# Kernel tuning notes

Hardware: AMD Instinct MI355X
Metric: run time of the kernel (lower is better)

## Reference

```python
import jax, jax.numpy as jnp
import numpy as np

HIDDEN = 1024
HEADS = 16
HEAD_DIM = HIDDEN // HEADS

def setup_inputs() -> dict:
    key = jax.random.key(0)
    k1, k2, k3 = jax.random.split(key, 3)
    scale = 1.0 / np.sqrt(HIDDEN)
    return {
        "x": jax.random.normal(k1, (2, 2048, HIDDEN), dtype=jnp.float32),
        "w_qkv": jax.random.normal(k2, (HIDDEN, 3 * HIDDEN), dtype=jnp.float32) * scale,
        "b_qkv": jnp.zeros((3 * HIDDEN,), dtype=jnp.float32),
        "w_out": jax.random.normal(k3, (HIDDEN, HIDDEN), dtype=jnp.float32) * scale,
        "b_out": jnp.zeros((HIDDEN,), dtype=jnp.float32),
    }

def reference(x, w_qkv, b_qkv, w_out, b_out):
    B, S, H = x.shape
    qkv = x @ w_qkv + b_qkv                              # (B,S,3H)
    qkv = qkv.reshape(B, S, 3, HEADS, HEAD_DIM)
    qkv = jnp.transpose(qkv, (2, 0, 3, 1, 4))            # (3,B,nh,S,hd)
    q, k, v = qkv[0], qkv[1], qkv[2]
    scores = jnp.einsum("bhqd,bhkd->bhqk", q, k) / np.sqrt(HEAD_DIM)
    causal = jnp.triu(jnp.ones((S, S), dtype=bool), k=1)  # True above diagonal
    scores = jnp.where(causal, -jnp.inf, scores)
    attn = jax.nn.softmax(scores, axis=-1)               # dropout: eval mode (identity)
    out = jnp.einsum("bhqk,bhkd->bhqd", attn, v)
    out = jnp.transpose(out, (0, 2, 1, 3)).reshape(B, S, H)
    return out @ w_out + b_out
```

## Files before the change

kernel.cpp:

```cpp
#include <hip/hip_runtime.h>
#include <hip/hip_bf16.h>

typedef short short8 __attribute__((ext_vector_type(8)));
typedef float f32x4 __attribute__((ext_vector_type(4)));
typedef unsigned int uint4v __attribute__((ext_vector_type(4)));

typedef const __attribute__((address_space(1))) unsigned int* gas_ptr;
typedef __attribute__((address_space(3))) unsigned int* las_ptr;
#define ASYNC16(g, l) __builtin_amdgcn_global_load_lds((gas_ptr)(g), (las_ptr)(l), 16, 0, 0)

__device__ __forceinline__ unsigned short f2bf(float f) {
    unsigned int u = __builtin_bit_cast(unsigned int, f);
    u += 0x7fff + ((u >> 16) & 1);
    return (unsigned short)(u >> 16);
}
__device__ __forceinline__ float bf2f(unsigned short s) {
    unsigned int u = (unsigned int)s << 16;
    return __builtin_bit_cast(float, u);
}
__device__ __forceinline__ unsigned int pkbf_trunc(float lo, float hi) {
    return __builtin_amdgcn_perm(__builtin_bit_cast(unsigned int, hi),
                                 __builtin_bit_cast(unsigned int, lo), 0x07060302u);
}
__device__ __forceinline__ float fexp2(float x) {
#if __has_builtin(__builtin_amdgcn_exp2f)
    return __builtin_amdgcn_exp2f(x);
#else
    return __expf(x * 0.6931471805599453f);
#endif
}

__device__ __forceinline__ void transpose_tile(
    const float* __restrict__ w, unsigned short* __restrict__ wt,
    int K, int N, int k0, int n0, unsigned short* tile)
{
    for (int i = threadIdx.x; i < 64 * 64; i += 256) {
        int r = i >> 6, c = i & 63;
        tile[r * 65 + c] = f2bf(w[(size_t)(k0 + r) * N + n0 + c]);
    }
    __syncthreads();
    for (int i = threadIdx.x; i < 64 * 64; i += 256) {
        int r = i >> 6, c = i & 63;
        wt[(size_t)(n0 + r) * K + k0 + c] = tile[c * 65 + r];
    }
}

__global__ __launch_bounds__(256) void prep(
    const float* __restrict__ x, const float* __restrict__ w_qkv,
    const float* __restrict__ w_out,
    unsigned short* __restrict__ x_b, unsigned short* __restrict__ wqkv_t,
    unsigned short* __restrict__ wout_t)
{
    __shared__ unsigned short tile[64 * 65];
    int bid = blockIdx.x;
    if (bid < 4096) {
        int i = (bid * 256 + threadIdx.x) * 4;
        float4 v = *(const float4*)(x + i);
        ushort4 o;
        o.x = f2bf(v.x); o.y = f2bf(v.y); o.z = f2bf(v.z); o.w = f2bf(v.w);
        *(ushort4*)(x_b + i) = o;
    } else if (bid < 4096 + 768) {
        int t = bid - 4096;
        transpose_tile(w_qkv, wqkv_t, 1024, 3072, (t / 48) * 64, (t % 48) * 64, tile);
    } else {
        int t = bid - 4864;
        transpose_tile(w_out, wout_t, 1024, 1024, (t >> 4) * 64, (t & 15) * 64, tile);
    }
}


template<bool OUT_BF16, bool QKV>
__global__ __launch_bounds__(256, 3) void gemm_bt(
    const unsigned short* __restrict__ A,
    const unsigned short* __restrict__ Bt,
    const float* __restrict__ bias,
    void* __restrict__ C,
    unsigned short* __restrict__ vTp,
    int M, int N, int K)
{
    __shared__ __align__(16) unsigned short As[2][128 * 32];
    __shared__ __align__(16) unsigned short Bs[2][128 * 32];
    const int tid = threadIdx.x;
    const int lane = tid & 63;
    const int wave = tid >> 6;
    const int wr = wave >> 1, wc = wave & 1;
    const int m0 = blockIdx.x * 128, n0 = blockIdx.y * 128;
    const int fr = lane & 15, fq = lane >> 4;

    f32x4 acc[4][4] = {};

    const int grow = lane >> 2;
    const int gcol = (lane & 3) * 8;
    const unsigned short* Ag = A  + (size_t)(m0 + wave * 32 + grow) * K + gcol;
    const unsigned short* Bg = Bt + (size_t)(n0 + wave * 32 + grow) * K + gcol;
    const int wb0 = (wave * 32) * 32;
    const int wb1 = (wave * 32 + 16) * 32;

    for (int k0 = 0; k0 < K; k0 += 64) {
        __syncthreads();
        ASYNC16(Ag + k0,               As[0] + wb0);
        ASYNC16(Ag + 16 * K + k0,      As[0] + wb1);
        ASYNC16(Bg + k0,               Bs[0] + wb0);
        ASYNC16(Bg + 16 * K + k0,      Bs[0] + wb1);
        ASYNC16(Ag + k0 + 32,          As[1] + wb0);
        ASYNC16(Ag + 16 * K + k0 + 32, As[1] + wb1);
        ASYNC16(Bg + k0 + 32,          Bs[1] + wb0);
        ASYNC16(Bg + 16 * K + k0 + 32, Bs[1] + wb1);
        __syncthreads();

#pragma unroll
        for (int h = 0; h < 2; h++) {
            short8 af[4], bfr[4];
#pragma unroll
            for (int i = 0; i < 4; i++)
                af[i] = *(const short8*)(As[h] + (wr * 64 + i * 16 + fr) * 32 + fq * 8);
#pragma unroll
            for (int j = 0; j < 4; j++)
                bfr[j] = *(const short8*)(Bs[h] + (wc * 64 + j * 16 + fr) * 32 + fq * 8);
#pragma unroll
            for (int i = 0; i < 4; i++)
#pragma unroll
                for (int j = 0; j < 4; j++)
                    acc[i][j] = __builtin_amdgcn_mfma_f32_16x16x32_bf16(af[i], bfr[j], acc[i][j], 0, 0, 0);
        }
    }

#pragma unroll
    for (int i = 0; i < 4; i++)
#pragma unroll
        for (int j = 0; j < 4; j++) {
            int col = n0 + wc * 64 + j * 16 + fr;
            float bv = bias[col];
            if (QKV && col >= 2048) {
                int hh = (col - 2048) >> 6, d = col & 63;
#pragma unroll
                for (int r = 0; r < 4; r++) {
                    int row = m0 + wr * 64 + i * 16 + fq * 4 + r;
                    int bb = row >> 11, s = row & 2047;
                    vTp[((size_t)(bb * 16 + hh) * 64 + d) * 2048 + s] = f2bf(acc[i][j][r] + bv);
                }
            } else {
                const int cstride = QKV ? 2048 : N;
#pragma unroll
                for (int r = 0; r < 4; r++) {
                    int row = m0 + wr * 64 + i * 16 + fq * 4 + r;
                    float v = acc[i][j][r] + bv;
                    if (OUT_BF16)
                        ((unsigned short*)C)[(size_t)row * cstride + col] = f2bf(v);
                    else
                        ((float*)C)[(size_t)row * cstride + col] = v;
                }
            }
        }
}


template<int RG0>
__device__ __forceinline__ void attn_step(
    const unsigned short* __restrict__ Ks0, const unsigned short* __restrict__ Ks1,
    const unsigned short* __restrict__ Vs0, const unsigned short* __restrict__ Vs1,
    unsigned short* __restrict__ Psw,
    const short8 (&qf)[2][2], const short8 ones,
    f32x4 (&o_acc)[2][4], f32x4 (&l_acc)[2],
    int j0, int fr, int fq,
    const int (&qrow0)[2], bool diagA, bool diagB)
{
    const int kpos = ((fq + (fr >> 1)) & 3) * 8;
    short8 kf[4][2];
#pragma unroll
    for (int t = 0; t < 4; t++) {
        kf[t][0] = *(const short8*)(Ks0 + (t * 16 + fr) * 32 + kpos);
        kf[t][1] = *(const short8*)(Ks1 + (t * 16 + fr) * 32 + kpos);
    }

    const float C1 = 0.18033688011112042f;
    const float C2 = -11.541560327111707f;

#pragma unroll
    for (int rg = RG0; rg < 2; rg++) {
        f32x4 s[4];
        __builtin_amdgcn_s_setprio(1);
#pragma unroll
        for (int t = 0; t < 4; t++) {
            s[t] = (f32x4){0.f, 0.f, 0.f, 0.f};
            s[t] = __builtin_amdgcn_mfma_f32_16x16x32_bf16(kf[t][0], qf[rg][0], s[t], 0, 0, 0);
            s[t] = __builtin_amdgcn_mfma_f32_16x16x32_bf16(kf[t][1], qf[rg][1], s[t], 0, 0, 0);
        }
        __builtin_amdgcn_s_setprio(0);
        const bool diag = (rg == 0) ? diagA : diagB;
        unsigned short* prow = Psw + rg * (16 * 64);
        const int qr = qrow0[rg] + fr;
        if (diag) {
#pragma unroll
            for (int t = 0; t < 4; t++) {
                const int kb = j0 + t * 16 + fq * 4;
                float p[4];
#pragma unroll
                for (int r = 0; r < 4; r++) {
                    float v = fexp2(s[t][r] * C1 + C2);
                    if (kb + r > qr) v = 0.f;
                    p[r] = v;
                }
                uint2 pk;
                pk.x = pkbf_trunc(p[0], p[1]);
                pk.y = pkbf_trunc(p[2], p[3]);
                const int blk = (t * 2 + (fq >> 1) + fr) & 7;
                *(uint2*)(prow + fr * 64 + blk * 8 + (fq & 1) * 4) = pk;
            }
        } else {
#pragma unroll
            for (int t = 0; t < 4; t++) {
                float p[4];
#pragma unroll
                for (int r = 0; r < 4; r++)
                    p[r] = fexp2(s[t][r] * C1 + C2);
                uint2 pk;
                pk.x = pkbf_trunc(p[0], p[1]);
                pk.y = pkbf_trunc(p[2], p[3]);
                const int blk = (t * 2 + (fq >> 1) + fr) & 7;
                *(uint2*)(prow + fr * 64 + blk * 8 + (fq & 1) * 4) = pk;
            }
        }
    }

#pragma unroll
    for (int ks = 0; ks < 2; ks++) {
        const unsigned short* Vsb = ks ? Vs1 : Vs0;
        const int colp = ((ks * 4 + fq + fr) & 7) * 8;
        short8 pf[2];
#pragma unroll
        for (int rg = RG0; rg < 2; rg++)
            pf[rg] = *(const short8*)(Psw + rg * (16 * 64) + fr * 64 + colp);
        __builtin_amdgcn_s_setprio(1);
#pragma unroll
        for (int t = 0; t < 4; t++) {
            short8 vf = *(const short8*)(Vsb + (t * 16 + fr) * 32 + kpos);
#pragma unroll
            for (int rg = RG0; rg < 2; rg++)
                o_acc[rg][t] = __builtin_amdgcn_mfma_f32_16x16x32_bf16(pf[rg], vf, o_acc[rg][t], 0, 0, 0);
        }
#pragma unroll
        for (int rg = RG0; rg < 2; rg++)
            l_acc[rg] = __builtin_amdgcn_mfma_f32_16x16x32_bf16(pf[rg], ones, l_acc[rg], 0, 0, 0);
        __builtin_amdgcn_s_setprio(0);
    }
}

__global__ __launch_bounds__(256, 2) void flash_attn(
    const unsigned short* __restrict__ qkv,
    const unsigned short* __restrict__ vT,
    unsigned short* __restrict__ Opart,
    float* __restrict__ lpart)
{
    const int p = blockIdx.x;
    const int g = blockIdx.y;
    const int h = blockIdx.z & 15, b = blockIdx.z >> 4;
    const int tid = threadIdx.x, wave = tid >> 6, lane = tid & 63;
    const int fr = lane & 15, fq = lane >> 4;
    const size_t RS = 2048;

    const unsigned short* Qb = qkv + (size_t)b * 2048 * RS + h * 64;
    const unsigned short* Kb = Qb + 1024;
    const unsigned short* Vt = vT + (size_t)(b * 16 + h) * 64 * 2048;

    __shared__ __align__(16) unsigned short Ks[2][64 * 32];
    __shared__ __align__(16) unsigned short Vs[2][64 * 32];
    __shared__ __align__(16) unsigned short Ps[4][2 * 16 * 64];

    short8 qf[2][2];
    int qrow0[2];
#pragma unroll
    for (int rg = 0; rg < 2; rg++) {
        int qt = (rg == 0) ? p : (31 - p);
        qrow0[rg] = qt * 64 + wave * 16;
        const unsigned short* qrow = Qb + (size_t)(qrow0[rg] + fr) * RS;
        qf[rg][0] = *(const short8*)(qrow + fq * 8);
        qf[rg][1] = *(const short8*)(qrow + 32 + fq * 8);
    }
    short8 ones;
#pragma unroll
    for (int e = 0; e < 8; e++) ones[e] = (short)0x3F80;

    f32x4 o_acc[2][4] = {};
    f32x4 l_acc[2] = {};

    const int grow = lane >> 2;
    const int gswz = (((lane & 3) - (grow >> 1)) & 3) * 8;
    const unsigned short* Kg = Kb + (size_t)(wave * 16 + grow) * RS + gswz;
    const unsigned short* Vg = Vt + (size_t)(wave * 16 + grow) * 2048 + gswz;
    const int wb = wave * 16 * 32;

    unsigned short* dK0 = Ks[0] + wb + lane * 8;
    unsigned short* dK1 = Ks[1] + wb + lane * 8;
    unsigned short* dV0 = Vs[0] + wb + lane * 8;
    unsigned short* dV1 = Vs[1] + wb + lane * 8;

    const int mid = (p >= 8) ? 8 : (16 - p);
    const int lo = g ? mid : 0;
    const int hi = g ? (32 - p) : mid;

    {
        const int j0 = lo * 64;
        uint4v aK0 = *(const uint4v*)(Kg + (size_t)j0 * RS);
        uint4v aK1 = *(const uint4v*)(Kg + (size_t)j0 * RS + 32);
        uint4v aV0 = *(const uint4v*)(Vg + j0);
        uint4v aV1 = *(const uint4v*)(Vg + j0 + 32);
        *(uint4v*)dK0 = aK0;
        *(uint4v*)dK1 = aK1;
        *(uint4v*)dV0 = aV0;
        *(uint4v*)dV1 = aV1;
    }
    __syncthreads();

    for (int jt = lo; jt < hi; jt++) {
        const int j0 = jt * 64;
        const bool more = (jt + 1 < hi);
        const int j0n = more ? (j0 + 64) : j0;

        uint4v aK0 = *(const uint4v*)(Kg + (size_t)j0n * RS);
        uint4v aK1 = *(const uint4v*)(Kg + (size_t)j0n * RS + 32);
        uint4v aV0 = *(const uint4v*)(Vg + j0n);
        uint4v aV1 = *(const uint4v*)(Vg + j0n + 32);

        bool diagA = (jt == p), diagB = (jt == 31 - p);
        if (jt <= p)
            attn_step<0>(Ks[0], Ks[1], Vs[0], Vs[1], Ps[wave], qf, ones,
                         o_acc, l_acc, j0, fr, fq, qrow0, diagA, diagB);
        else
            attn_step<1>(Ks[0], Ks[1], Vs[0], Vs[1], Ps[wave], qf, ones,
                         o_acc, l_acc, j0, fr, fq, qrow0, diagA, diagB);

        __syncthreads();
        if (more) {
            *(uint4v*)dK0 = aK0;
            *(uint4v*)dK1 = aK1;
            *(uint4v*)dV0 = aV0;
            *(uint4v*)dV1 = aV1;
        }
        __syncthreads();
    }

    unsigned short* Og = Opart + (size_t)g * 4096 * 1024;
    float* lg = lpart + (size_t)g * 4096 * 16;
#pragma unroll
    for (int rg = 0; rg < 2; rg++) {
#pragma unroll
        for (int t = 0; t < 4; t++)
#pragma unroll
            for (int r = 0; r < 4; r++) {
                int row = qrow0[rg] + fq * 4 + r;
                Og[(size_t)(b * 2048 + row) * 1024 + h * 64 + t * 16 + fr] = f2bf(o_acc[rg][t][r]);
            }
        if (fr == 0) {
#pragma unroll
            for (int r = 0; r < 4; r++) {
                int row = qrow0[rg] + fq * 4 + r;
                lg[(size_t)(b * 2048 + row) * 16 + h] = l_acc[rg][r];
            }
        }
    }
}

__global__ __launch_bounds__(256) void reduce_attn(
    const unsigned short* __restrict__ Opart, const float* __restrict__ lpart,
    unsigned short* __restrict__ out)
{
    int i = (blockIdx.x * 256 + threadIdx.x) * 8;
    int row = i >> 10, h = (i & 1023) >> 6;
    float lsum = lpart[(size_t)row * 16 + h] + lpart[(size_t)4096 * 16 + row * 16 + h];
    float inv = 1.0f / lsum;
    ushort4 a0 = *(const ushort4*)(Opart + i);
    ushort4 a1 = *(const ushort4*)(Opart + i + 4);
    ushort4 b0 = *(const ushort4*)(Opart + (size_t)4096 * 1024 + i);
    ushort4 b1 = *(const ushort4*)(Opart + (size_t)4096 * 1024 + i + 4);
    ushort4 o0, o1;
    o0.x = f2bf((bf2f(a0.x) + bf2f(b0.x)) * inv);
    o0.y = f2bf((bf2f(a0.y) + bf2f(b0.y)) * inv);
    o0.z = f2bf((bf2f(a0.z) + bf2f(b0.z)) * inv);
    o0.w = f2bf((bf2f(a0.w) + bf2f(b0.w)) * inv);
    o1.x = f2bf((bf2f(a1.x) + bf2f(b1.x)) * inv);
    o1.y = f2bf((bf2f(a1.y) + bf2f(b1.y)) * inv);
    o1.z = f2bf((bf2f(a1.z) + bf2f(b1.z)) * inv);
    o1.w = f2bf((bf2f(a1.w) + bf2f(b1.w)) * inv);
    *(ushort4*)(out + i) = o0;
    *(ushort4*)(out + i + 4) = o1;
}

extern "C" void kernel_launch(void* const* d_in, const int* in_sizes, int n_in,
                              void* d_out, int out_size, void* d_ws, size_t ws_size,
                              hipStream_t stream) {
    const float* x      = (const float*)d_in[0];
    const float* w_qkv  = (const float*)d_in[1];
    const float* b_qkv  = (const float*)d_in[2];
    const float* w_out  = (const float*)d_in[3];
    const float* b_out  = (const float*)d_in[4];
    float* out = (float*)d_out;

    char* ws = (char*)d_ws;
    unsigned short* x_b    = (unsigned short*)(ws);
    unsigned short* wqkv_t = (unsigned short*)(ws + 8u  * 1024 * 1024);
    unsigned short* wout_t = (unsigned short*)(ws + 14u * 1024 * 1024);
    unsigned short* qkv    = (unsigned short*)(ws + 16u * 1024 * 1024);
    unsigned short* attn   = (unsigned short*)(ws + 32u * 1024 * 1024);
    unsigned short* vT     = (unsigned short*)(ws + 40u * 1024 * 1024);
    unsigned short* Opart  = (unsigned short*)(ws + 48u * 1024 * 1024);
    float*          lpart  = (float*)         (ws + 64u * 1024 * 1024);

    prep<<<5120, 256, 0, stream>>>(x, w_qkv, w_out, x_b, wqkv_t, wout_t);
    gemm_bt<true, true ><<<dim3(32, 24), 256, 0, stream>>>(x_b,  wqkv_t, b_qkv, qkv, vT, 4096, 3072, 1024);
    flash_attn<<<dim3(16, 2, 32), 256, 0, stream>>>(qkv, vT, Opart, lpart);
    reduce_attn<<<2048, 256, 0, stream>>>(Opart, lpart, attn);
    gemm_bt<false, false><<<dim3(32, 8),  256, 0, stream>>>(attn, wout_t, b_out, out, nullptr, 4096, 1024, 1024);
}
```

Before: 187.4 us.

## Fuse x bf16 conversion and attention-split reduction into GEMM A-operand loads

The GEMM A-tile loading now reads fp32 x directly and converts it to bf16 in registers. It also combines the two flash-attention partial outputs and normalises them by the summed l values before writing into LDS. This removes the x-conversion portion of prep and the separate reduce_attn kernel, cutting a launch and a bf16 round trip through global memory. The cost is that A loads become synchronous register loads instead of async global-to-LDS copies. The QKV GEMM (24 column blocks) re-converts x redundantly, and the output GEMM (8 column blocks) re-reads two partials plus l values and redoes the divide.

```diff
diff --git a/kernel.cpp b/kernel.cpp
--- a/kernel.cpp
+++ b/kernel.cpp
@@ -17,6 +17,9 @@
 __device__ __forceinline__ float bf2f(unsigned short s) {
     unsigned int u = (unsigned int)s << 16;
     return __builtin_bit_cast(float, u);
+}
+__device__ __forceinline__ unsigned int pack2bf(float lo, float hi) {
+    return (unsigned int)f2bf(lo) | ((unsigned int)f2bf(hi) << 16);
 }
 __device__ __forceinline__ unsigned int pkbf_trunc(float lo, float hi) {
     return __builtin_amdgcn_perm(__builtin_bit_cast(unsigned int, hi),
@@ -46,34 +49,26 @@
 }
 
 __global__ __launch_bounds__(256) void prep(
-    const float* __restrict__ x, const float* __restrict__ w_qkv,
-    const float* __restrict__ w_out,
-    unsigned short* __restrict__ x_b, unsigned short* __restrict__ wqkv_t,
-    unsigned short* __restrict__ wout_t)
+    const float* __restrict__ w_qkv, const float* __restrict__ w_out,
+    unsigned short* __restrict__ wqkv_t, unsigned short* __restrict__ wout_t)
 {
     __shared__ unsigned short tile[64 * 65];
     int bid = blockIdx.x;
-    if (bid < 4096) {
-        int i = (bid * 256 + threadIdx.x) * 4;
-        float4 v = *(const float4*)(x + i);
-        ushort4 o;
-        o.x = f2bf(v.x); o.y = f2bf(v.y); o.z = f2bf(v.z); o.w = f2bf(v.w);
-        *(ushort4*)(x_b + i) = o;
-    } else if (bid < 4096 + 768) {
-        int t = bid - 4096;
-        transpose_tile(w_qkv, wqkv_t, 1024, 3072, (t / 48) * 64, (t % 48) * 64, tile);
+    if (bid < 768) {
+        transpose_tile(w_qkv, wqkv_t, 1024, 3072, (bid / 48) * 64, (bid % 48) * 64, tile);
     } else {
-        int t = bid - 4864;
+        int t = bid - 768;
         transpose_tile(w_out, wout_t, 1024, 1024, (t >> 4) * 64, (t & 15) * 64, tile);
     }
 }
 
 
-template<bool OUT_BF16, bool QKV>
+template<int AMODE, bool OUT_BF16, bool QKV>
 __global__ __launch_bounds__(256, 3) void gemm_bt(
-    const unsigned short* __restrict__ A,
+    const void* __restrict__ Araw,
     const unsigned short* __restrict__ Bt,
     const float* __restrict__ bias,
+    const float* __restrict__ lp,
     void* __restrict__ C,
     unsigned short* __restrict__ vTp,
     int M, int N, int K)
@@ -91,21 +86,57 @@
 
     const int grow = lane >> 2;
     const int gcol = (lane & 3) * 8;
-    const unsigned short* Ag = A  + (size_t)(m0 + wave * 32 + grow) * K + gcol;
-    const unsigned short* Bg = Bt + (size_t)(n0 + wave * 32 + grow) * K + gcol;
+    const int lrow = wave * 32 + grow;
+    const unsigned short* Bg = Bt + (size_t)(n0 + lrow) * K + gcol;
     const int wb0 = (wave * 32) * 32;
     const int wb1 = (wave * 32 + 16) * 32;
 
     for (int k0 = 0; k0 < K; k0 += 64) {
         __syncthreads();
-        ASYNC16(Ag + k0,               As[0] + wb0);
-        ASYNC16(Ag + 16 * K + k0,      As[0] + wb1);
         ASYNC16(Bg + k0,               Bs[0] + wb0);
         ASYNC16(Bg + 16 * K + k0,      Bs[0] + wb1);
-        ASYNC16(Ag + k0 + 32,          As[1] + wb0);
-        ASYNC16(Ag + 16 * K + k0 + 32, As[1] + wb1);
         ASYNC16(Bg + k0 + 32,          Bs[1] + wb0);
         ASYNC16(Bg + 16 * K + k0 + 32, Bs[1] + wb1);
+#pragma unroll
+        for (int h2 = 0; h2 < 2; h2++) {
+            const int r  = lrow + h2 * 16;
+            const int gr = m0 + r;
+#pragma unroll
+            for (int tw = 0; tw < 2; tw++) {
+                const int cb = k0 + tw * 32 + gcol;
+                uint4v w;
+                if (AMODE == 1) {
+                    const float* Af = (const float*)Araw;
+                    const float* src = Af + (size_t)gr * K + cb;
+                    float4 v0 = *(const float4*)src;
+                    float4 v1 = *(const float4*)(src + 4);
+                    w[0] = pack2bf(v0.x, v0.y);
+                    w[1] = pack2bf(v0.z, v0.w);
+                    w[2] = pack2bf(v1.x, v1.y);
+                    w[3] = pack2bf(v1.z, v1.w);
+                } else {
+                    const unsigned short* O0 = (const unsigned short*)Araw;
+                    const unsigned short* O1 = O0 + (size_t)4096 * 1024;
+                    const int hcol = cb >> 6;
+                    float ls = lp[(size_t)gr * 16 + hcol]
+                             + lp[(size_t)4096 * 16 + gr * 16 + hcol];
+                    float inv = 1.0f / ls;
+                    ushort4 a0 = *(const ushort4*)(O0 + (size_t)gr * 1024 + cb);
+                    ushort4 a1 = *(const ushort4*)(O0 + (size_t)gr * 1024 + cb + 4);
+                    ushort4 b0 = *(const ushort4*)(O1 + (size_t)gr * 1024 + cb);
+                    ushort4 b1 = *(const ushort4*)(O1 + (size_t)gr * 1024 + cb + 4);
+                    w[0] = pack2bf((bf2f(a0.x) + bf2f(b0.x)) * inv,
+                                   (bf2f(a0.y) + bf2f(b0.y)) * inv);
+                    w[1] = pack2bf((bf2f(a0.z) + bf2f(b0.z)) * inv,
+                                   (bf2f(a0.w) + bf2f(b0.w)) * inv);
+                    w[2] = pack2bf((bf2f(a1.x) + bf2f(b1.x)) * inv,
+                                   (bf2f(a1.y) + bf2f(b1.y)) * inv);
+                    w[3] = pack2bf((bf2f(a1.z) + bf2f(b1.z)) * inv,
+                                   (bf2f(a1.w) + bf2f(b1.w)) * inv);
+                }
+                *(uint4v*)(As[tw] + r * 32 + gcol) = w;
+            }
+        }
         __syncthreads();
 
 #pragma unroll
@@ -361,31 +392,6 @@
     }
 }
 
-__global__ __launch_bounds__(256) void reduce_attn(
-    const unsigned short* __restrict__ Opart, const float* __restrict__ lpart,
-    unsigned short* __restrict__ out)
-{
-    int i = (blockIdx.x * 256 + threadIdx.x) * 8;
-    int row = i >> 10, h = (i & 1023) >> 6;
-    float lsum = lpart[(size_t)row * 16 + h] + lpart[(size_t)4096 * 16 + row * 16 + h];
-    float inv = 1.0f / lsum;
-    ushort4 a0 = *(const ushort4*)(Opart + i);
-    ushort4 a1 = *(const ushort4*)(Opart + i + 4);
-    ushort4 b0 = *(const ushort4*)(Opart + (size_t)4096 * 1024 + i);
-    ushort4 b1 = *(const ushort4*)(Opart + (size_t)4096 * 1024 + i + 4);
-    ushort4 o0, o1;
-    o0.x = f2bf((bf2f(a0.x) + bf2f(b0.x)) * inv);
-    o0.y = f2bf((bf2f(a0.y) + bf2f(b0.y)) * inv);
-    o0.z = f2bf((bf2f(a0.z) + bf2f(b0.z)) * inv);
-    o0.w = f2bf((bf2f(a0.w) + bf2f(b0.w)) * inv);
-    o1.x = f2bf((bf2f(a1.x) + bf2f(b1.x)) * inv);
-    o1.y = f2bf((bf2f(a1.y) + bf2f(b1.y)) * inv);
-    o1.z = f2bf((bf2f(a1.z) + bf2f(b1.z)) * inv);
-    o1.w = f2bf((bf2f(a1.w) + bf2f(b1.w)) * inv);
-    *(ushort4*)(out + i) = o0;
-    *(ushort4*)(out + i + 4) = o1;
-}
-
 extern "C" void kernel_launch(void* const* d_in, const int* in_sizes, int n_in,
                               void* d_out, int out_size, void* d_ws, size_t ws_size,
                               hipStream_t stream) {
@@ -397,18 +403,15 @@
     float* out = (float*)d_out;
 
     char* ws = (char*)d_ws;
-    unsigned short* x_b    = (unsigned short*)(ws);
     unsigned short* wqkv_t = (unsigned short*)(ws + 8u  * 1024 * 1024);
     unsigned short* wout_t = (unsigned short*)(ws + 14u * 1024 * 1024);
     unsigned short* qkv    = (unsigned short*)(ws + 16u * 1024 * 1024);
-    unsigned short* attn   = (unsigned short*)(ws + 32u * 1024 * 1024);
     unsigned short* vT     = (unsigned short*)(ws + 40u * 1024 * 1024);
     unsigned short* Opart  = (unsigned short*)(ws + 48u * 1024 * 1024);
     float*          lpart  = (float*)         (ws + 64u * 1024 * 1024);
 
-    prep<<<5120, 256, 0, stream>>>(x, w_qkv, w_out, x_b, wqkv_t, wout_t);
-    gemm_bt<true, true ><<<dim3(32, 24), 256, 0, stream>>>(x_b,  wqkv_t, b_qkv, qkv, vT, 4096, 3072, 1024);
+    prep<<<1024, 256, 0, stream>>>(w_qkv, w_out, wqkv_t, wout_t);
+    gemm_bt<1, true, true ><<<dim3(32, 24), 256, 0, stream>>>(x, wqkv_t, b_qkv, nullptr, qkv, vT, 4096, 3072, 1024);
     flash_attn<<<dim3(16, 2, 32), 256, 0, stream>>>(qkv, vT, Opart, lpart);
-    reduce_attn<<<2048, 256, 0, stream>>>(Opart, lpart, attn);
-    gemm_bt<false, false><<<dim3(32, 8),  256, 0, stream>>>(attn, wout_t, b_out, out, nullptr, 4096, 1024, 1024);
-}
+    gemm_bt<2, false, false><<<dim3(32, 8), 256, 0, stream>>>(Opart, wout_t, b_out, lpart, out, nullptr, 4096, 1024, 1024);
+}
```

Result: slower. 219.8 us (+17.3%).

## Remove split-KV partitioning and fuse normalization into flash attention epilogue

Applied to the files above, without the earlier changes.

Each attention block now processes the full causal key range for its paired query tiles instead of splitting it into two halves. The separate reduction kernel and the partial O/l buffers are removed, and the output is normalized by 1/l directly in the epilogue. This avoids the partial writes, the extra launch and the reduce pass, at the cost of half as many blocks and longer per-block serial loops.

```diff
diff --git a/kernel.cpp b/kernel.cpp
--- a/kernel.cpp
+++ b/kernel.cpp
@@ -249,12 +249,10 @@
 __global__ __launch_bounds__(256, 2) void flash_attn(
     const unsigned short* __restrict__ qkv,
     const unsigned short* __restrict__ vT,
-    unsigned short* __restrict__ Opart,
-    float* __restrict__ lpart)
+    unsigned short* __restrict__ attn)
 {
     const int p = blockIdx.x;
-    const int g = blockIdx.y;
-    const int h = blockIdx.z & 15, b = blockIdx.z >> 4;
+    const int h = blockIdx.y & 15, b = blockIdx.y >> 4;
     const int tid = threadIdx.x, wave = tid >> 6, lane = tid & 63;
     const int fr = lane & 15, fq = lane >> 4;
     const size_t RS = 2048;
@@ -295,16 +293,13 @@
     unsigned short* dV0 = Vs[0] + wb + lane * 8;
     unsigned short* dV1 = Vs[1] + wb + lane * 8;
 
-    const int mid = (p >= 8) ? 8 : (16 - p);
-    const int lo = g ? mid : 0;
-    const int hi = g ? (32 - p) : mid;
+    const int hi = 32 - p;
 
     {
-        const int j0 = lo * 64;
-        uint4v aK0 = *(const uint4v*)(Kg + (size_t)j0 * RS);
-        uint4v aK1 = *(const uint4v*)(Kg + (size_t)j0 * RS + 32);
-        uint4v aV0 = *(const uint4v*)(Vg + j0);
-        uint4v aV1 = *(const uint4v*)(Vg + j0 + 32);
+        uint4v aK0 = *(const uint4v*)(Kg);
+        uint4v aK1 = *(const uint4v*)(Kg + 32);
+        uint4v aV0 = *(const uint4v*)(Vg);
+        uint4v aV1 = *(const uint4v*)(Vg + 32);
         *(uint4v*)dK0 = aK0;
         *(uint4v*)dK1 = aK1;
         *(uint4v*)dV0 = aV0;
@@ -312,7 +307,7 @@
     }
     __syncthreads();
 
-    for (int jt = lo; jt < hi; jt++) {
+    for (int jt = 0; jt < hi; jt++) {
         const int j0 = jt * 64;
         const bool more = (jt + 1 < hi);
         const int j0n = more ? (j0 + 64) : j0;
@@ -340,50 +335,21 @@
         __syncthreads();
     }
 
-    unsigned short* Og = Opart + (size_t)g * 4096 * 1024;
-    float* lg = lpart + (size_t)g * 4096 * 16;
 #pragma unroll
     for (int rg = 0; rg < 2; rg++) {
+        float inv[4];
+#pragma unroll
+        for (int r = 0; r < 4; r++)
+            inv[r] = 1.0f / l_acc[rg][r];
 #pragma unroll
         for (int t = 0; t < 4; t++)
 #pragma unroll
             for (int r = 0; r < 4; r++) {
                 int row = qrow0[rg] + fq * 4 + r;
-                Og[(size_t)(b * 2048 + row) * 1024 + h * 64 + t * 16 + fr] = f2bf(o_acc[rg][t][r]);
+                attn[(size_t)(b * 2048 + row) * 1024 + h * 64 + t * 16 + fr] =
+                    f2bf(o_acc[rg][t][r] * inv[r]);
             }
-        if (fr == 0) {
-#pragma unroll
-            for (int r = 0; r < 4; r++) {
-                int row = qrow0[rg] + fq * 4 + r;
-                lg[(size_t)(b * 2048 + row) * 16 + h] = l_acc[rg][r];
-            }
-        }
-    }
-}
-
-__global__ __launch_bounds__(256) void reduce_attn(
-    const unsigned short* __restrict__ Opart, const float* __restrict__ lpart,
-    unsigned short* __restrict__ out)
-{
-    int i = (blockIdx.x * 256 + threadIdx.x) * 8;
-    int row = i >> 10, h = (i & 1023) >> 6;
-    float lsum = lpart[(size_t)row * 16 + h] + lpart[(size_t)4096 * 16 + row * 16 + h];
-    float inv = 1.0f / lsum;
-    ushort4 a0 = *(const ushort4*)(Opart + i);
-    ushort4 a1 = *(const ushort4*)(Opart + i + 4);
-    ushort4 b0 = *(const ushort4*)(Opart + (size_t)4096 * 1024 + i);
-    ushort4 b1 = *(const ushort4*)(Opart + (size_t)4096 * 1024 + i + 4);
-    ushort4 o0, o1;
-    o0.x = f2bf((bf2f(a0.x) + bf2f(b0.x)) * inv);
-    o0.y = f2bf((bf2f(a0.y) + bf2f(b0.y)) * inv);
-    o0.z = f2bf((bf2f(a0.z) + bf2f(b0.z)) * inv);
-    o0.w = f2bf((bf2f(a0.w) + bf2f(b0.w)) * inv);
-    o1.x = f2bf((bf2f(a1.x) + bf2f(b1.x)) * inv);
-    o1.y = f2bf((bf2f(a1.y) + bf2f(b1.y)) * inv);
-    o1.z = f2bf((bf2f(a1.z) + bf2f(b1.z)) * inv);
-    o1.w = f2bf((bf2f(a1.w) + bf2f(b1.w)) * inv);
-    *(ushort4*)(out + i) = o0;
-    *(ushort4*)(out + i + 4) = o1;
+    }
 }
 
 extern "C" void kernel_launch(void* const* d_in, const int* in_sizes, int n_in,
@@ -403,12 +369,9 @@
     unsigned short* qkv    = (unsigned short*)(ws + 16u * 1024 * 1024);
     unsigned short* attn   = (unsigned short*)(ws + 32u * 1024 * 1024);
     unsigned short* vT     = (unsigned short*)(ws + 40u * 1024 * 1024);
-    unsigned short* Opart  = (unsigned short*)(ws + 48u * 1024 * 1024);
-    float*          lpart  = (float*)         (ws + 64u * 1024 * 1024);
 
     prep<<<5120, 256, 0, stream>>>(x, w_qkv, w_out, x_b, wqkv_t, wout_t);
     gemm_bt<true, true ><<<dim3(32, 24), 256, 0, stream>>>(x_b,  wqkv_t, b_qkv, qkv, vT, 4096, 3072, 1024);
-    flash_attn<<<dim3(16, 2, 32), 256, 0, stream>>>(qkv, vT, Opart, lpart);
-    reduce_attn<<<2048, 256, 0, stream>>>(Opart, lpart, attn);
+    flash_attn<<<dim3(16, 32), 256, 0, stream>>>(qkv, vT, attn);
     gemm_bt<false, false><<<dim3(32, 8),  256, 0, stream>>>(attn, wout_t, b_out, out, nullptr, 4096, 1024, 1024);
 }
```

Result: faster. 173.3 us (median of 2 runs) (-7.5%).
